# Kernel optimization log

Measured on AMD Instinct MI355X. Metric: run time of the kernel, lower is better.

The kernel has to match this reference:

```python
import jax, jax.numpy as jnp
import numpy as np

H, I, E, TOPK = 2048, 4096, 8, 2
B, S = 2, 2048

def setup_inputs() -> dict:
    key = jax.random.key(0)
    ks = jax.random.split(key, 6)
    x = jax.random.normal(ks[0], (B, S, H), dtype=jnp.float32)
    expert_indices = jax.random.randint(ks[1], (B, S, TOPK), 0, E, dtype=jnp.int64)
    expert_weights = jax.random.uniform(ks[2], (B, S, TOPK), dtype=jnp.float32)
    gate_proj = jax.random.normal(ks[3], (E, I, H), dtype=jnp.float32) * 0.02
    up_proj = jax.random.normal(ks[4], (E, I, H), dtype=jnp.float32) * 0.02
    down_proj = jax.random.normal(ks[5], (E, H, I), dtype=jnp.float32) * 0.02
    return {"x": x, "expert_indices": expert_indices, "expert_weights": expert_weights,
            "gate_proj": gate_proj, "up_proj": up_proj, "down_proj": down_proj}

def reference(x, expert_indices, expert_weights, gate_proj, up_proj, down_proj):
    b, s, h = x.shape
    T = b * s
    xf = x.reshape(T, h)                                   # [T, H]
    idx = expert_indices.reshape(T, -1)                    # [T, K]
    w = expert_weights.reshape(T, -1)                      # [T, K]
    n_exp = gate_proj.shape[0]
    # Per-token combined weight for each expert (sums duplicate slots, matching
    # the original weighted scatter-add over (token, slot) pairs).
    onehot = jax.nn.one_hot(idx, n_exp, dtype=xf.dtype)    # [T, K, E]
    we = jnp.einsum('tk,tke->et', w, onehot)               # [E, T]

    def step(acc, inp):
        g_w, u_w, d_w, w_e = inp                           # [I,H], [I,H], [H,I], [T]
        g = xf @ g_w.T                                     # [T, I]
        u = xf @ u_w.T                                     # [T, I]
        inter = g * jax.nn.sigmoid(g) * u                  # fused SiLU(g) * u
        acc = acc + w_e[:, None] * (inter @ d_w.T)         # weighted combine
        return acc, None

    out0 = jnp.zeros((T, h), dtype=x.dtype)
    out, _ = jax.lax.scan(step, out0, (gate_proj, up_proj, down_proj, we))
    return out.reshape(b, s, h)
```

## Files before the change

kernel.cpp:

```cpp
#include <hip/hip_runtime.h>
#include <hip/hip_bf16.h>
#include <stdint.h>

#define H_DIM 2048
#define I_DIM 4096
#define NEXP  8
#define NTOK  4096
#define NPAIR 8192
#define PAD_ROWS (NPAIR + 256)

#define MiB (1024ull * 1024ull)
#define WS_COUNTS   0ull
#define WS_OFFSETS  256ull
#define WS_TOKID    1024ull
#define WS_SLOT     (64ull * 1024)
#define WS_PAIRW    (128ull * 1024)
#define WS_XG       (1ull * MiB)
#define WS_INTER    (36ull * MiB)
#define WS_Y        (104ull * MiB)
#define WS_GW       (176ull * MiB)
#define WS_UW       (304ull * MiB)
#define WS_DW       (432ull * MiB)
#define WS_FULL     (560ull * MiB)

typedef __attribute__((ext_vector_type(8))) short bf16x8;
typedef __attribute__((ext_vector_type(4))) float f32x4;

#if defined(__has_builtin)
#if __has_builtin(__builtin_amdgcn_cvt_pk_bf16_f32)
#define HAVE_CVT_PK 1
#endif
#endif

__device__ __forceinline__ uint32_t bf16_bits_rne(float x) {
  uint32_t u = __float_as_uint(x);
  return (u + 0x7FFFu + ((u >> 16) & 1u)) >> 16;
}
__device__ __forceinline__ uint32_t pk_bf16(float a, float b) {
#ifdef HAVE_CVT_PK
  auto r = __builtin_amdgcn_cvt_pk_bf16_f32(a, b);
  return __builtin_bit_cast(uint32_t, r);
#else
  return bf16_bits_rne(a) | (bf16_bits_rne(b) << 16);
#endif
}
__device__ __forceinline__ uint16_t bf16_one(float x) {
  return (uint16_t)(pk_bf16(x, x) & 0xFFFFu);
}

__device__ __forceinline__ void async_load16(const void* g, void* l) {
  __builtin_amdgcn_global_load_lds(
      (const __attribute__((address_space(1))) void*)g,
      (__attribute__((address_space(3))) void*)l, 16, 0, 0);
}

#define WAIT_VM6()  do { asm volatile("s_waitcnt vmcnt(6)" ::: "memory"); __builtin_amdgcn_sched_barrier(0); } while (0)
#define WAIT_VM0()  do { asm volatile("s_waitcnt vmcnt(0)" ::: "memory"); __builtin_amdgcn_sched_barrier(0); } while (0)
#define BARRIER()   do { __builtin_amdgcn_s_barrier(); asm volatile("" ::: "memory"); } while (0)

__global__ void route_kernel(const int* __restrict__ idx, const float* __restrict__ wts,
                             int* __restrict__ ws_counts, int* __restrict__ ws_offsets,
                             int* __restrict__ tokid, int* __restrict__ slotOf,
                             float* __restrict__ pairw) {
  __shared__ int s_cnt[NEXP], s_off[NEXP], s_cur[NEXP];
  int tid = threadIdx.x;
  if (tid < NEXP) s_cnt[tid] = 0;
  __syncthreads();
  for (int p = tid; p < NPAIR; p += 256) atomicAdd(&s_cnt[idx[p]], 1);
  __syncthreads();
  if (tid == 0) {
    int acc = 0;
    for (int e = 0; e < NEXP; e++) { s_off[e] = acc; s_cur[e] = acc; acc += s_cnt[e]; }
  }
  __syncthreads();
  for (int p = tid; p < NPAIR; p += 256) {
    int e = idx[p];
    int slot = atomicAdd(&s_cur[e], 1);
    tokid[slot] = p >> 1;
    slotOf[p] = slot;
    pairw[slot] = wts[p];
  }
  if (tid < NEXP) { ws_counts[tid] = s_cnt[tid]; ws_offsets[tid] = s_off[tid]; }
}

__global__ void gather_cast_kernel(const float* __restrict__ x, const int* __restrict__ tokid,
                                   uint16_t* __restrict__ xg) {
  int p = blockIdx.x;
  int t = tokid[p];
  int c = threadIdx.x * 8;
  const float4* src = (const float4*)(x + (size_t)t * H_DIM + c);
  float4 v0 = src[0], v1 = src[1];
  uint4 o;
  o.x = pk_bf16(v0.x, v0.y); o.y = pk_bf16(v0.z, v0.w);
  o.z = pk_bf16(v1.x, v1.y); o.w = pk_bf16(v1.z, v1.w);
  *(uint4*)(xg + (size_t)p * H_DIM + c) = o;
}

__global__ void cast3_kernel(const float* __restrict__ g, const float* __restrict__ u,
                             const float* __restrict__ d,
                             uint16_t* __restrict__ gw, uint16_t* __restrict__ uw,
                             uint16_t* __restrict__ dw) {
  const float* src = blockIdx.y == 0 ? g : (blockIdx.y == 1 ? u : d);
  uint16_t*    dst = blockIdx.y == 0 ? gw : (blockIdx.y == 1 ? uw : dw);
  const long long n8 = (long long)NEXP * I_DIM * H_DIM / 8;
  long long stride = (long long)gridDim.x * blockDim.x;
  for (long long i = (long long)blockIdx.x * blockDim.x + threadIdx.x; i < n8; i += stride) {
    const float4* s = (const float4*)(src + i * 8);
    float4 a = s[0], b = s[1];
    uint4 o = { pk_bf16(a.x, a.y), pk_bf16(a.z, a.w), pk_bf16(b.x, b.y), pk_bf16(b.z, b.w) };
    *(uint4*)(dst + i * 8) = o;
  }
}

#define T1_A    (256 * 64)
#define T1_B    (64 * 64)
#define T1_ELE  (T1_A + 2 * T1_B)

__global__ __launch_bounds__(512, 1)
void gemm1_v2(const uint16_t* __restrict__ xg,
              const uint16_t* __restrict__ gw, const uint16_t* __restrict__ uw,
              const int* __restrict__ ws_counts, const int* __restrict__ ws_offsets,
              uint16_t* __restrict__ inter) {
  int e = blockIdx.z;
  int cnt = ws_counts[e];
  int rowTile = blockIdx.y;
  if (rowTile * 256 >= cnt) return;
  int off = ws_offsets[e];
  int colBase = blockIdx.x * 64;
  size_t rowBase = (size_t)off + (size_t)rowTile * 256;

  __shared__ uint16_t lds[3 * T1_ELE];

  int tid = threadIdx.x, lane = tid & 63, w = tid >> 6;
  int r8 = lane >> 3;
  int gsw = ((lane & 7) ^ r8) << 3;

  const uint16_t* srcA[4];
#pragma unroll
  for (int c = 0; c < 4; c++)
    srcA[c] = xg + (rowBase + (size_t)(w * 32 + c * 8 + r8)) * H_DIM + gsw;
  const uint16_t* srcG = gw + ((size_t)e * I_DIM + colBase + w * 8 + r8) * H_DIM + gsw;
  const uint16_t* srcU = uw + ((size_t)e * I_DIM + colBase + w * 8 + r8) * H_DIM + gsw;

  const int dA = w * 2048;
  const int dG = T1_A + w * 512;
  const int dU = T1_A + T1_B + w * 512;

  f32x4 accg[4][2], accu[4][2];
  f32x4 zero = {0.f, 0.f, 0.f, 0.f};
#pragma unroll
  for (int mi = 0; mi < 4; mi++)
#pragma unroll
    for (int ni = 0; ni < 2; ni++) { accg[mi][ni] = zero; accu[mi][ni] = zero; }

  auto STG = [&](int kt, int b) {
    uint16_t* lb = lds + b * T1_ELE;
    int ko = kt * 64;
#pragma unroll
    for (int c = 0; c < 4; c++) async_load16(srcA[c] + ko, lb + dA + c * 512);
    async_load16(srcG + ko, lb + dG);
    async_load16(srcU + ko, lb + dU);
  };

  STG(0, 0); STG(1, 1);
  WAIT_VM6();
  BARRIER();

  int wr = w >> 1, wc = w & 1;
  int wm = wr * 64, wn = wc * 32;
  int lcol = lane & 15, quad = lane >> 4;
  int sx = (lcol & 7) << 3;

  const int NT = H_DIM / 64;
  for (int t = 0; t < NT; ++t) {
    if (t + 2 < NT) STG(t + 2, (t + 2) % 3);
    const uint16_t* lb = lds + (t % 3) * T1_ELE;
#pragma unroll
    for (int ks = 0; ks < 2; ks++) {
      int krs = (ks * 32 + quad * 8) ^ sx;
      bf16x8 af[4], bg_[2], bu_[2];
#pragma unroll
      for (int mi = 0; mi < 4; mi++)
        af[mi] = *(const bf16x8*)(lb + (wm + mi * 16 + lcol) * 64 + krs);
#pragma unroll
      for (int ni = 0; ni < 2; ni++) {
        bg_[ni] = *(const bf16x8*)(lb + T1_A + (wn + ni * 16 + lcol) * 64 + krs);
        bu_[ni] = *(const bf16x8*)(lb + T1_A + T1_B + (wn + ni * 16 + lcol) * 64 + krs);
      }
      __builtin_amdgcn_s_setprio(1);
#pragma unroll
      for (int mi = 0; mi < 4; mi++)
#pragma unroll
        for (int ni = 0; ni < 2; ni++) {
          accg[mi][ni] = __builtin_amdgcn_mfma_f32_16x16x32_bf16(af[mi], bg_[ni], accg[mi][ni], 0, 0, 0);
          accu[mi][ni] = __builtin_amdgcn_mfma_f32_16x16x32_bf16(af[mi], bu_[ni], accu[mi][ni], 0, 0, 0);
        }
      __builtin_amdgcn_s_setprio(0);
    }
    if (t + 2 < NT) { WAIT_VM6(); } else { WAIT_VM0(); }
    BARRIER();
  }

  int col0 = colBase + wn;
#pragma unroll
  for (int mi = 0; mi < 4; mi++) {
#pragma unroll
    for (int r = 0; r < 4; r++) {
      int localRow = rowTile * 256 + wm + mi * 16 + quad * 4 + r;
      if (localRow < cnt) {
        size_t prow = (size_t)off + localRow;
#pragma unroll
        for (int ni = 0; ni < 2; ni++) {
          float g = accg[mi][ni][r], u = accu[mi][ni][r];
          float v = (g / (1.f + __expf(-g))) * u;
          inter[prow * I_DIM + col0 + ni * 16 + lcol] = bf16_one(v);
        }
      }
    }
  }
}

#define T2_A    (256 * 64)
#define T2_B    (128 * 64)
#define T2_ELE  (T2_A + T2_B)

__global__ __launch_bounds__(512, 1)
void gemm2_v2(const uint16_t* __restrict__ inter, const uint16_t* __restrict__ dw,
              const int* __restrict__ ws_counts, const int* __restrict__ ws_offsets,
              const float* __restrict__ pairw, float* __restrict__ y) {
  int e = blockIdx.z;
  int cnt = ws_counts[e];
  int rowTile = blockIdx.y;
  if (rowTile * 256 >= cnt) return;
  int off = ws_offsets[e];
  int colBase = blockIdx.x * 128;
  size_t rowBase = (size_t)off + (size_t)rowTile * 256;

  __shared__ uint16_t lds[3 * T2_ELE];

  int tid = threadIdx.x, lane = tid & 63, w = tid >> 6;
  int r8 = lane >> 3;
  int gsw = ((lane & 7) ^ r8) << 3;

  const uint16_t* srcA[4];
#pragma unroll
  for (int c = 0; c < 4; c++)
    srcA[c] = inter + (rowBase + (size_t)(w * 32 + c * 8 + r8)) * I_DIM + gsw;
  const uint16_t* srcB[2];
#pragma unroll
  for (int c = 0; c < 2; c++)
    srcB[c] = dw + ((size_t)e * H_DIM + colBase + w * 16 + c * 8 + r8) * I_DIM + gsw;

  const int dA = w * 2048;
  const int dB = T2_A + w * 1024;

  f32x4 acc[4][4];
  f32x4 zero = {0.f, 0.f, 0.f, 0.f};
#pragma unroll
  for (int mi = 0; mi < 4; mi++)
#pragma unroll
    for (int ni = 0; ni < 4; ni++) acc[mi][ni] = zero;

  auto STG = [&](int kt, int b) {
    uint16_t* lb = lds + b * T2_ELE;
    int ko = kt * 64;
#pragma unroll
    for (int c = 0; c < 4; c++) async_load16(srcA[c] + ko, lb + dA + c * 512);
#pragma unroll
    for (int c = 0; c < 2; c++) async_load16(srcB[c] + ko, lb + dB + c * 512);
  };

  STG(0, 0); STG(1, 1);
  WAIT_VM6();
  BARRIER();

  int wr = w >> 1, wc = w & 1;
  int wm = wr * 64, wn = wc * 64;
  int lcol = lane & 15, quad = lane >> 4;
  int sx = (lcol & 7) << 3;

  const int NT = I_DIM / 64;
  for (int t = 0; t < NT; ++t) {
    if (t + 2 < NT) STG(t + 2, (t + 2) % 3);
    const uint16_t* lb = lds + (t % 3) * T2_ELE;
#pragma unroll
    for (int ks = 0; ks < 2; ks++) {
      int krs = (ks * 32 + quad * 8) ^ sx;
      bf16x8 af[4], bf_[4];
#pragma unroll
      for (int mi = 0; mi < 4; mi++)
        af[mi] = *(const bf16x8*)(lb + (wm + mi * 16 + lcol) * 64 + krs);
#pragma unroll
      for (int ni = 0; ni < 4; ni++)
        bf_[ni] = *(const bf16x8*)(lb + T2_A + (wn + ni * 16 + lcol) * 64 + krs);
      __builtin_amdgcn_s_setprio(1);
#pragma unroll
      for (int mi = 0; mi < 4; mi++)
#pragma unroll
        for (int ni = 0; ni < 4; ni++)
          acc[mi][ni] = __builtin_amdgcn_mfma_f32_16x16x32_bf16(af[mi], bf_[ni], acc[mi][ni], 0, 0, 0);
      __builtin_amdgcn_s_setprio(0);
    }
    if (t + 2 < NT) { WAIT_VM6(); } else { WAIT_VM0(); }
    BARRIER();
  }

  int col0 = colBase + wn;
#pragma unroll
  for (int mi = 0; mi < 4; mi++) {
#pragma unroll
    for (int r = 0; r < 4; r++) {
      int localRow = rowTile * 256 + wm + mi * 16 + quad * 4 + r;
      if (localRow < cnt) {
        size_t prow = (size_t)off + localRow;
        float wgt = pairw[prow];
        float* yr = y + prow * H_DIM + col0;
#pragma unroll
        for (int ni = 0; ni < 4; ni++)
          yr[ni * 16 + lcol] = acc[mi][ni][r] * wgt;
      }
    }
  }
}

__global__ void combine_kernel(const float* __restrict__ y, const int* __restrict__ slotOf,
                               float* __restrict__ out) {
  int t = blockIdx.x;
  int s0 = slotOf[2 * t], s1 = slotOf[2 * t + 1];
  int c = threadIdx.x * 8;
  const float4* a = (const float4*)(y + (size_t)s0 * H_DIM + c);
  const float4* b = (const float4*)(y + (size_t)s1 * H_DIM + c);
  float4 a0 = a[0], a1 = a[1], b0 = b[0], b1 = b[1];
  float4 o0 = {a0.x + b0.x, a0.y + b0.y, a0.z + b0.z, a0.w + b0.w};
  float4 o1 = {a1.x + b1.x, a1.y + b1.y, a1.z + b1.z, a1.w + b1.w};
  float4* dst = (float4*)(out + (size_t)t * H_DIM + c);
  dst[0] = o0; dst[1] = o1;
}

extern "C" void kernel_launch(void* const* d_in, const int* in_sizes, int n_in,
                              void* d_out, int out_size, void* d_ws, size_t ws_size,
                              hipStream_t stream) {
  const float* x    = (const float*)d_in[0];
  const int*   eidx = (const int*)d_in[1];
  const float* ew   = (const float*)d_in[2];
  const float* gate = (const float*)d_in[3];
  const float* up   = (const float*)d_in[4];
  const float* down = (const float*)d_in[5];
  float* out = (float*)d_out;
  char* ws = (char*)d_ws;

  if (ws_size < WS_FULL) {
    hipMemsetAsync(d_out, 0, (size_t)NTOK * H_DIM * sizeof(float), stream);
    return;
  }

  int*      counts  = (int*)(ws + WS_COUNTS);
  int*      offsets = (int*)(ws + WS_OFFSETS);
  int*      tokid   = (int*)(ws + WS_TOKID);
  int*      slotOf  = (int*)(ws + WS_SLOT);
  float*    pairw   = (float*)(ws + WS_PAIRW);
  uint16_t* xg      = (uint16_t*)(ws + WS_XG);
  uint16_t* inter   = (uint16_t*)(ws + WS_INTER);
  float*    y       = (float*)(ws + WS_Y);
  uint16_t* gw      = (uint16_t*)(ws + WS_GW);
  uint16_t* uw      = (uint16_t*)(ws + WS_UW);
  uint16_t* dwp     = (uint16_t*)(ws + WS_DW);

  route_kernel<<<1, 256, 0, stream>>>(eidx, ew, counts, offsets, tokid, slotOf, pairw);
  gather_cast_kernel<<<NPAIR, 256, 0, stream>>>(x, tokid, xg);
  cast3_kernel<<<dim3(2048, 3), 256, 0, stream>>>(gate, up, down, gw, uw, dwp);

  gemm1_v2<<<dim3(I_DIM / 64, NPAIR / 256, NEXP), 512, 0, stream>>>(
      xg, gw, uw, counts, offsets, inter);
  gemm2_v2<<<dim3(H_DIM / 128, NPAIR / 256, NEXP), 512, 0, stream>>>(
      inter, dwp, counts, offsets, pairw, y);
  combine_kernel<<<NTOK, 256, 0, stream>>>(y, slotOf, out);
}
```

Measured before the change: 1.333 ms.

## Interleave async global-to-LDS prefetch with MFMA half-steps in both MoE GEMMs

Both expert GEMM kernels now split each K-tile into two explicit half-steps. The async global-to-LDS prefetch for tile t+2 is divided into two groups of three loads, issued between the LDS fragment reads and the MFMA block of each half. Barriers and lgkmcnt waits are placed around each half so that memory issue interleaves with matrix compute rather than being front-loaded. The intent is a finer-grained schedule that hides load latency better, at the cost of extra barriers per K-tile.

```diff
diff --git a/kernel.cpp b/kernel.cpp
--- a/kernel.cpp
+++ b/kernel.cpp
@@ -54,9 +54,10 @@
       (__attribute__((address_space(3))) void*)l, 16, 0, 0);
 }
 
-#define WAIT_VM6()  do { asm volatile("s_waitcnt vmcnt(6)" ::: "memory"); __builtin_amdgcn_sched_barrier(0); } while (0)
-#define WAIT_VM0()  do { asm volatile("s_waitcnt vmcnt(0)" ::: "memory"); __builtin_amdgcn_sched_barrier(0); } while (0)
-#define BARRIER()   do { __builtin_amdgcn_s_barrier(); asm volatile("" ::: "memory"); } while (0)
+#define WAIT_VM6()   do { asm volatile("s_waitcnt vmcnt(6)" ::: "memory"); __builtin_amdgcn_sched_barrier(0); } while (0)
+#define WAIT_VM0()   do { asm volatile("s_waitcnt vmcnt(0)" ::: "memory"); __builtin_amdgcn_sched_barrier(0); } while (0)
+#define WAIT_LGKM0() do { asm volatile("s_waitcnt lgkmcnt(0)" ::: "memory"); __builtin_amdgcn_sched_barrier(0); } while (0)
+#define BARRIER()    do { __builtin_amdgcn_s_barrier(); asm volatile("" ::: "memory"); } while (0)
 
 __global__ void route_kernel(const int* __restrict__ idx, const float* __restrict__ wts,
                              int* __restrict__ ws_counts, int* __restrict__ ws_offsets,
@@ -117,7 +118,7 @@
 #define T1_ELE  (T1_A + 2 * T1_B)
 
 __global__ __launch_bounds__(512, 1)
-void gemm1_v2(const uint16_t* __restrict__ xg,
+void gemm1_v5(const uint16_t* __restrict__ xg,
               const uint16_t* __restrict__ gw, const uint16_t* __restrict__ uw,
               const int* __restrict__ ws_counts, const int* __restrict__ ws_offsets,
               uint16_t* __restrict__ inter) {
@@ -153,6 +154,11 @@
 #pragma unroll
     for (int ni = 0; ni < 2; ni++) { accg[mi][ni] = zero; accu[mi][ni] = zero; }
 
+  int wr = w >> 1, wc = w & 1;
+  int wm = wr * 64, wn = wc * 32;
+  int lcol = lane & 15, quad = lane >> 4;
+  int sx = (lcol & 7) << 3;
+
   auto STG = [&](int kt, int b) {
     uint16_t* lb = lds + b * T1_ELE;
     int ko = kt * 64;
@@ -166,18 +172,16 @@
   WAIT_VM6();
   BARRIER();
 
-  int wr = w >> 1, wc = w & 1;
-  int wm = wr * 64, wn = wc * 32;
-  int lcol = lane & 15, quad = lane >> 4;
-  int sx = (lcol & 7) << 3;
-
   const int NT = H_DIM / 64;
   for (int t = 0; t < NT; ++t) {
-    if (t + 2 < NT) STG(t + 2, (t + 2) % 3);
-    const uint16_t* lb = lds + (t % 3) * T1_ELE;
-#pragma unroll
-    for (int ks = 0; ks < 2; ks++) {
-      int krs = (ks * 32 + quad * 8) ^ sx;
+    const int b = t % 3, b2 = (t + 2) % 3;
+    uint16_t* lb  = lds + b * T1_ELE;
+    uint16_t* lb2 = lds + b2 * T1_ELE;
+    const bool pre = (t + 2 < NT);
+    const int ko = (t + 2) * 64;
+
+    {
+      const int krs = (quad * 8) ^ sx;
       bf16x8 af[4], bg_[2], bu_[2];
 #pragma unroll
       for (int mi = 0; mi < 4; mi++)
@@ -187,6 +191,13 @@
         bg_[ni] = *(const bf16x8*)(lb + T1_A + (wn + ni * 16 + lcol) * 64 + krs);
         bu_[ni] = *(const bf16x8*)(lb + T1_A + T1_B + (wn + ni * 16 + lcol) * 64 + krs);
       }
+      if (pre) {
+        async_load16(srcA[0] + ko, lb2 + dA + 0 * 512);
+        async_load16(srcA[1] + ko, lb2 + dA + 1 * 512);
+        async_load16(srcA[2] + ko, lb2 + dA + 2 * 512);
+      }
+      BARRIER();
+      WAIT_LGKM0();
       __builtin_amdgcn_s_setprio(1);
 #pragma unroll
       for (int mi = 0; mi < 4; mi++)
@@ -196,9 +207,38 @@
           accu[mi][ni] = __builtin_amdgcn_mfma_f32_16x16x32_bf16(af[mi], bu_[ni], accu[mi][ni], 0, 0, 0);
         }
       __builtin_amdgcn_s_setprio(0);
-    }
-    if (t + 2 < NT) { WAIT_VM6(); } else { WAIT_VM0(); }
-    BARRIER();
+      BARRIER();
+    }
+    {
+      const int krs = (32 + quad * 8) ^ sx;
+      bf16x8 af[4], bg_[2], bu_[2];
+#pragma unroll
+      for (int mi = 0; mi < 4; mi++)
+        af[mi] = *(const bf16x8*)(lb + (wm + mi * 16 + lcol) * 64 + krs);
+#pragma unroll
+      for (int ni = 0; ni < 2; ni++) {
+        bg_[ni] = *(const bf16x8*)(lb + T1_A + (wn + ni * 16 + lcol) * 64 + krs);
+        bu_[ni] = *(const bf16x8*)(lb + T1_A + T1_B + (wn + ni * 16 + lcol) * 64 + krs);
+      }
+      if (pre) {
+        async_load16(srcA[3] + ko, lb2 + dA + 3 * 512);
+        async_load16(srcG + ko, lb2 + dG);
+        async_load16(srcU + ko, lb2 + dU);
+      }
+      BARRIER();
+      WAIT_LGKM0();
+      __builtin_amdgcn_s_setprio(1);
+#pragma unroll
+      for (int mi = 0; mi < 4; mi++)
+#pragma unroll
+        for (int ni = 0; ni < 2; ni++) {
+          accg[mi][ni] = __builtin_amdgcn_mfma_f32_16x16x32_bf16(af[mi], bg_[ni], accg[mi][ni], 0, 0, 0);
+          accu[mi][ni] = __builtin_amdgcn_mfma_f32_16x16x32_bf16(af[mi], bu_[ni], accu[mi][ni], 0, 0, 0);
+        }
+      __builtin_amdgcn_s_setprio(0);
+      if (pre) { WAIT_VM6(); } else { WAIT_VM0(); }
+      BARRIER();
+    }
   }
 
   int col0 = colBase + wn;
@@ -225,7 +265,7 @@
 #define T2_ELE  (T2_A + T2_B)
 
 __global__ __launch_bounds__(512, 1)
-void gemm2_v2(const uint16_t* __restrict__ inter, const uint16_t* __restrict__ dw,
+void gemm2_v5(const uint16_t* __restrict__ inter, const uint16_t* __restrict__ dw,
               const int* __restrict__ ws_counts, const int* __restrict__ ws_offsets,
               const float* __restrict__ pairw, float* __restrict__ y) {
   int e = blockIdx.z;
@@ -261,48 +301,83 @@
 #pragma unroll
     for (int ni = 0; ni < 4; ni++) acc[mi][ni] = zero;
 
-  auto STG = [&](int kt, int b) {
-    uint16_t* lb = lds + b * T2_ELE;
-    int ko = kt * 64;
-#pragma unroll
-    for (int c = 0; c < 4; c++) async_load16(srcA[c] + ko, lb + dA + c * 512);
-#pragma unroll
-    for (int c = 0; c < 2; c++) async_load16(srcB[c] + ko, lb + dB + c * 512);
-  };
-
-  STG(0, 0); STG(1, 1);
-  WAIT_VM6();
-  BARRIER();
-
   int wr = w >> 1, wc = w & 1;
   int wm = wr * 64, wn = wc * 64;
   int lcol = lane & 15, quad = lane >> 4;
   int sx = (lcol & 7) << 3;
 
+  auto STG = [&](int kt, int b) {
+    uint16_t* lb = lds + b * T2_ELE;
+    int ko = kt * 64;
+#pragma unroll
+    for (int c = 0; c < 4; c++) async_load16(srcA[c] + ko, lb + dA + c * 512);
+#pragma unroll
+    for (int c = 0; c < 2; c++) async_load16(srcB[c] + ko, lb + dB + c * 512);
+  };
+
+  STG(0, 0); STG(1, 1);
+  WAIT_VM6();
+  BARRIER();
+
   const int NT = I_DIM / 64;
   for (int t = 0; t < NT; ++t) {
-    if (t + 2 < NT) STG(t + 2, (t + 2) % 3);
-    const uint16_t* lb = lds + (t % 3) * T2_ELE;
-#pragma unroll
-    for (int ks = 0; ks < 2; ks++) {
-      int krs = (ks * 32 + quad * 8) ^ sx;
-      bf16x8 af[4], bf_[4];
+    const int b = t % 3, b2 = (t + 2) % 3;
+    uint16_t* lb  = lds + b * T2_ELE;
+    uint16_t* lb2 = lds + b2 * T2_ELE;
+    const bool pre = (t + 2 < NT);
+    const int ko = (t + 2) * 64;
+
+    {
+      const int krs = (quad * 8) ^ sx;
+      bf16x8 af[4], bb[4];
 #pragma unroll
       for (int mi = 0; mi < 4; mi++)
         af[mi] = *(const bf16x8*)(lb + (wm + mi * 16 + lcol) * 64 + krs);
 #pragma unroll
       for (int ni = 0; ni < 4; ni++)
-        bf_[ni] = *(const bf16x8*)(lb + T2_A + (wn + ni * 16 + lcol) * 64 + krs);
+        bb[ni] = *(const bf16x8*)(lb + T2_A + (wn + ni * 16 + lcol) * 64 + krs);
+      if (pre) {
+        async_load16(srcA[0] + ko, lb2 + dA + 0 * 512);
+        async_load16(srcA[1] + ko, lb2 + dA + 1 * 512);
+        async_load16(srcA[2] + ko, lb2 + dA + 2 * 512);
+      }
+      BARRIER();
+      WAIT_LGKM0();
       __builtin_amdgcn_s_setprio(1);
 #pragma unroll
       for (int mi = 0; mi < 4; mi++)
 #pragma unroll
         for (int ni = 0; ni < 4; ni++)
-          acc[mi][ni] = __builtin_amdgcn_mfma_f32_16x16x32_bf16(af[mi], bf_[ni], acc[mi][ni], 0, 0, 0);
+          acc[mi][ni] = __builtin_amdgcn_mfma_f32_16x16x32_bf16(af[mi], bb[ni], acc[mi][ni], 0, 0, 0);
       __builtin_amdgcn_s_setprio(0);
-    }
-    if (t + 2 < NT) { WAIT_VM6(); } else { WAIT_VM0(); }
-    BARRIER();
+      BARRIER();
+    }
+    {
+      const int krs = (32 + quad * 8) ^ sx;
+      bf16x8 af[4], bb[4];
+#pragma unroll
+      for (int mi = 0; mi < 4; mi++)
+        af[mi] = *(const bf16x8*)(lb + (wm + mi * 16 + lcol) * 64 + krs);
+#pragma unroll
+      for (int ni = 0; ni < 4; ni++)
+        bb[ni] = *(const bf16x8*)(lb + T2_A + (wn + ni * 16 + lcol) * 64 + krs);
+      if (pre) {
+        async_load16(srcA[3] + ko, lb2 + dA + 3 * 512);
+        async_load16(srcB[0] + ko, lb2 + dB + 0 * 512);
+        async_load16(srcB[1] + ko, lb2 + dB + 1 * 512);
+      }
+      BARRIER();
+      WAIT_LGKM0();
+      __builtin_amdgcn_s_setprio(1);
+#pragma unroll
+      for (int mi = 0; mi < 4; mi++)
+#pragma unroll
+        for (int ni = 0; ni < 4; ni++)
+          acc[mi][ni] = __builtin_amdgcn_mfma_f32_16x16x32_bf16(af[mi], bb[ni], acc[mi][ni], 0, 0, 0);
+      __builtin_amdgcn_s_setprio(0);
+      if (pre) { WAIT_VM6(); } else { WAIT_VM0(); }
+      BARRIER();
+    }
   }
 
   int col0 = colBase + wn;
@@ -370,9 +445,9 @@
   gather_cast_kernel<<<NPAIR, 256, 0, stream>>>(x, tokid, xg);
   cast3_kernel<<<dim3(2048, 3), 256, 0, stream>>>(gate, up, down, gw, uw, dwp);
 
-  gemm1_v2<<<dim3(I_DIM / 64, NPAIR / 256, NEXP), 512, 0, stream>>>(
+  gemm1_v5<<<dim3(I_DIM / 64, NPAIR / 256, NEXP), 512, 0, stream>>>(
       xg, gw, uw, counts, offsets, inter);
-  gemm2_v2<<<dim3(H_DIM / 128, NPAIR / 256, NEXP), 512, 0, stream>>>(
+  gemm2_v5<<<dim3(H_DIM / 128, NPAIR / 256, NEXP), 512, 0, stream>>>(
       inter, dwp, counts, offsets, pairw, y);
   combine_kernel<<<NTOK, 256, 0, stream>>>(y, slotOf, out);
 }
```

After: 1.312 ms. Within noise of the previous version (-1.6%).
